# Kernel tuning notes

Hardware: AMD Instinct MI355X
Metric: run time of the kernel (lower is better)

## Reference

```python
import jax, jax.numpy as jnp
import numpy as np

B, T, D = 32, 4096, 768
HEADS, DK, DV = 4, 64, 64
REL_W = 32
HIDDEN = 256


def setup_inputs() -> dict:
    key = jax.random.key(0)
    ks = jax.random.split(key, 12)
    H_sent = jax.random.normal(ks[0], (B, T, D), dtype=jnp.float32)
    # realistic padding: each sample has a random valid length in [2048, T]
    lengths = jax.random.randint(ks[1], (B,), 2048, T + 1)
    attention_mask_sent = (jnp.arange(T)[None, :] < lengths[:, None]).astype(jnp.int32)
    noun_pos = jax.random.randint(ks[2], (B,), 0, 2048).astype(jnp.int32)
    pooled_fields = jax.random.normal(ks[3], (B, D), dtype=jnp.float32)
    # xavier-uniform for (heads, d, dk): fan_in=d, fan_out=dk per torch semantics
    def xavier(k, shape, fan_in, fan_out):
        lim = float(np.sqrt(6.0 / (fan_in + fan_out)))
        return jax.random.uniform(k, shape, jnp.float32, -lim, lim)
    WQ = xavier(ks[4], (HEADS, D, DK), D, DK)
    WK = xavier(ks[5], (HEADS, D, DK), D, DK)
    WV = xavier(ks[6], (HEADS, D, DV), D, DV)
    rel_bias = jnp.zeros((HEADS, 2 * REL_W + 1), jnp.float32) + 0.01 * jax.random.normal(ks[7], (HEADS, 2 * REL_W + 1))
    in_proj = D + HEADS * DV + D  # 1792
    proj_w = xavier(ks[8], (HIDDEN, in_proj), in_proj, HIDDEN)
    proj_b = jnp.zeros((HIDDEN,), jnp.float32)
    mlp_w = xavier(ks[9], (2, HIDDEN), HIDDEN, 2)
    mlp_b = jnp.zeros((2,), jnp.float32)
    return {
        "H_sent": H_sent, "attention_mask_sent": attention_mask_sent,
        "noun_pos": noun_pos, "pooled_fields": pooled_fields,
        "WQ": WQ, "WK": WK, "WV": WV, "rel_bias": rel_bias,
        "proj_w": proj_w, "proj_b": proj_b, "mlp_w": mlp_w, "mlp_b": mlp_b,
    }


def reference(H_sent, attention_mask_sent, noun_pos, pooled_fields,
              WQ, WK, WV, rel_bias, proj_w, proj_b, mlp_w, mlp_b):
    b, t, d = H_sent.shape
    heads, _, dk = WQ.shape
    w = (rel_bias.shape[1] - 1) // 2
    # gather single query vector per sample
    h_i = H_sent[jnp.arange(b), noun_pos]  # (B, d)
    Q = jnp.einsum('bd,hdk->bhk', h_i, WQ)        # (B, H, dk)
    K = jnp.einsum('btd,hdk->bthk', H_sent, WK)   # (B, T, H, dk)
    V = jnp.einsum('btd,hdv->bthv', H_sent, WV)   # (B, T, H, dv)
    scores = jnp.einsum('bhk,bthk->bht', Q, K) / jnp.sqrt(jnp.float32(dk))  # (B,H,T)
    # relative-position bias gathered by clamped delta
    delta = jnp.clip(jnp.arange(t)[None, :] - noun_pos[:, None], -w, w) + w  # (B,T)
    rb = rel_bias[:, delta]                        # (H, B, T)
    scores = scores + jnp.transpose(rb, (1, 0, 2))
    scores = jnp.where(attention_mask_sent[:, None, :] == 0, jnp.float32(-1e9), scores)
    alpha = jax.nn.softmax(scores, axis=-1)        # (B, H, T)
    c = jnp.einsum('bht,bthv->bhv', alpha, V).reshape(b, -1)  # (B, H*dv)
    r = jnp.concatenate([h_i, c, pooled_fields], axis=-1)     # (B, d + H*dv + d)
    hdn = jax.nn.gelu(r @ proj_w.T + proj_b, approximate=False)
    logits = hdn @ mlp_w.T + mlp_b                 # (B, 2)
    return logits
```

## Files before the change

kernel.cpp:

```cpp
#include <hip/hip_runtime.h>
#include <math.h>

#define BB 32
#define TT 4096
#define DD 768
#define NH 4
#define RELW 32
#define NREL 65
#define HIDDEN 256
#define INPROJ 1792

#define NCH 32
#define CROWS (TT / NCH)
#define TROWS 8
#define NT (CROWS / TROWS)
#define C4 (DD / 4)

#define BARRIER() __builtin_amdgcn_s_barrier()
#define FENCE_LGKM() asm volatile("s_waitcnt lgkmcnt(0)" ::: "memory")
#define WAITVM6() asm volatile("s_waitcnt vmcnt(6)" ::: "memory")
#define WAITVM0() asm volatile("s_waitcnt vmcnt(0)" ::: "memory")

__device__ __forceinline__ void gl_lds16(const float* g, float* l) {
    __builtin_amdgcn_global_load_lds(
        (const __attribute__((address_space(1))) float*)(uintptr_t)g,
        (__attribute__((address_space(3))) float*)(uintptr_t)l,
        16, 0, 0);
}

__global__ __launch_bounds__(256) void kA(const float* __restrict__ H,
                                          const int* __restrict__ noun_pos,
                                          const float* __restrict__ WQ,
                                          const float* __restrict__ WK,
                                          float* __restrict__ R,
                                          float* __restrict__ qk_ws) {
    int b = blockIdx.x / NH, h = blockIdx.x % NH;
    __shared__ float hi_s[DD];
    __shared__ float q_s[64];
    int tn = noun_pos[b];
    const float* Hrow = H + ((size_t)b * TT + tn) * DD;
    for (int d = threadIdx.x; d < DD; d += 256) {
        float v = Hrow[d];
        hi_s[d] = v;
        if (h == 0) R[(size_t)b * INPROJ + d] = v;
    }
    __syncthreads();
    if (threadIdx.x < 64) {
        int k = threadIdx.x;
        const float* wq = WQ + (size_t)h * DD * 64 + k;
        float acc = 0.f;
        for (int d = 0; d < DD; ++d) acc += hi_s[d] * wq[(size_t)d * 64];
        q_s[k] = acc;
    }
    __syncthreads();
    for (int d = threadIdx.x; d < DD; d += 256) {
        const float* wk = WK + ((size_t)h * DD + d) * 64;
        float acc = 0.f;
        #pragma unroll
        for (int k = 0; k < 64; ++k) acc += q_s[k] * wk[k];
        qk_ws[((size_t)b * NH + h) * DD + d] = acc * 0.125f;
    }
}

__global__ __launch_bounds__(256, 2) void kFlash(const float* __restrict__ H,
                                                 const int* __restrict__ mask,
                                                 const int* __restrict__ noun_pos,
                                                 const float* __restrict__ rel_bias,
                                                 const float* __restrict__ qk_ws,
                                                 float* __restrict__ macc,
                                                 float* __restrict__ ml) {
    const int b   = blockIdx.x / NCH;
    const int ch  = blockIdx.x % NCH;
    const int tid = threadIdx.x;
    const int wave = tid >> 6, lane = tid & 63;
    const int sl = lane >> 2, hh = lane & 3;

    __shared__ float4 Hts[2][TROWS * C4];
    __shared__ float4 rbL[CROWS];
    __shared__ __align__(16) float sL[TROWS * NH];
    __shared__ int snl;

    const int t0 = ch * CROWS;
    const int tn = noun_pos[b];

    if (tid == 0) snl = 0;
    __syncthreads();

    if (tid < CROWS) {
        int t = t0 + tid;
        int dl = t - tn; dl = dl < -RELW ? -RELW : (dl > RELW ? RELW : dl);
        int mm = mask[(size_t)b * TT + t];
        float4 rv;
        if (mm) {
            rv.x = rel_bias[0 * NREL + dl + RELW];
            rv.y = rel_bias[1 * NREL + dl + RELW];
            rv.z = rel_bias[2 * NREL + dl + RELW];
            rv.w = rel_bias[3 * NREL + dl + RELW];
            atomicMax(&snl, tid + 1);
        } else {
            rv.x = rv.y = rv.z = rv.w = -2.0e9f;
        }
        rbL[tid] = rv;
    }

    float4 qkr[12];
    {
        const float4* qk4 = (const float4*)(qk_ws + ((size_t)b * NH + hh) * DD);
        #pragma unroll
        for (int j = 0; j < 12; ++j) qkr[j] = qk4[j * 16 + sl];
    }

    __syncthreads();
    const int NTE = (snl + TROWS - 1) / TROWS;

    if (NTE == 0) {
        float4 z = {0.f, 0.f, 0.f, 0.f};
        if (tid < C4) {
            float4* mo = (float4*)(macc + (size_t)blockIdx.x * NH * DD);
            mo[0 * C4 + tid] = z; mo[1 * C4 + tid] = z;
            mo[2 * C4 + tid] = z; mo[3 * C4 + tid] = z;
        }
        if (tid == 0) {
            float* mp = ml + (size_t)blockIdx.x * NH * 2;
            mp[0] = -3.0e38f; mp[1] = 0.f; mp[2] = -3.0e38f; mp[3] = 0.f;
            mp[4] = -3.0e38f; mp[5] = 0.f; mp[6] = -3.0e38f; mp[7] = 0.f;
        }
        return;
    }

    float m0 = -3.0e38f, m1 = -3.0e38f, m2 = -3.0e38f, m3 = -3.0e38f;
    float l0 = 0.f, l1 = 0.f, l2 = 0.f, l3 = 0.f;
    float4 a0 = {0.f,0.f,0.f,0.f}, a1 = {0.f,0.f,0.f,0.f};
    float4 a2 = {0.f,0.f,0.f,0.f}, a3 = {0.f,0.f,0.f,0.f};

    const float* Hc = H + ((size_t)b * TT + t0) * DD;

    {
        float* dst = (float*)&Hts[0][0];
        #pragma unroll
        for (int i = 0; i < 6; ++i) {
            int base = (wave * 6 + i) * 256;
            gl_lds16(Hc + base + lane * 4, dst + base);
        }
    }

    #pragma unroll 1
    for (int t = 0; t < NTE; ++t) {
        const int cur = t & 1;
        if (t + 1 < NTE) {
            const float* src = Hc + (size_t)(t + 1) * TROWS * DD;
            float* dst = (float*)&Hts[cur ^ 1][0];
            #pragma unroll
            for (int i = 0; i < 6; ++i) {
                int base = (wave * 6 + i) * 256;
                gl_lds16(src + base + lane * 4, dst + base);
            }
            WAITVM6();
        } else {
            WAITVM0();
        }
        BARRIER();

        const float4* Htc = &Hts[cur][0];
        #pragma unroll
        for (int k = 0; k < 2; ++k) {
            const int r = wave * 2 + k;
            const float4* Hr = Htc + r * C4;
            float acc = 0.f;
            #pragma unroll
            for (int j = 0; j < 12; ++j) {
                float4 hv = Hr[j * 16 + sl];
                acc += hv.x * qkr[j].x + hv.y * qkr[j].y + hv.z * qkr[j].z + hv.w * qkr[j].w;
            }
            acc += __shfl_xor(acc, 4);
            acc += __shfl_xor(acc, 8);
            acc += __shfl_xor(acc, 16);
            acc += __shfl_xor(acc, 32);
            if (lane < NH)
                sL[r * NH + lane] = acc + ((const float*)&rbL[t * TROWS + r])[lane];
        }
        FENCE_LGKM();
        BARRIER();

        float4 p4[TROWS];
        {
            const float4* sL4 = (const float4*)sL;
            #pragma unroll
            for (int r = 0; r < TROWS; ++r) p4[r] = sL4[r];
            float tx = p4[0].x, ty = p4[0].y, tz = p4[0].z, tw = p4[0].w;
            #pragma unroll
            for (int r = 1; r < TROWS; ++r) {
                tx = fmaxf(tx, p4[r].x); ty = fmaxf(ty, p4[r].y);
                tz = fmaxf(tz, p4[r].z); tw = fmaxf(tw, p4[r].w);
            }
            float n0 = fmaxf(m0, tx), n1 = fmaxf(m1, ty);
            float n2 = fmaxf(m2, tz), n3 = fmaxf(m3, tw);
            float s0 = __expf(m0 - n0), s1 = __expf(m1 - n1);
            float s2 = __expf(m2 - n2), s3 = __expf(m3 - n3);
            float q0 = 0.f, q1 = 0.f, q2 = 0.f, q3 = 0.f;
            #pragma unroll
            for (int r = 0; r < TROWS; ++r) {
                p4[r].x = __expf(p4[r].x - n0); q0 += p4[r].x;
                p4[r].y = __expf(p4[r].y - n1); q1 += p4[r].y;
                p4[r].z = __expf(p4[r].z - n2); q2 += p4[r].z;
                p4[r].w = __expf(p4[r].w - n3); q3 += p4[r].w;
            }
            l0 = l0 * s0 + q0; l1 = l1 * s1 + q1;
            l2 = l2 * s2 + q2; l3 = l3 * s3 + q3;
            m0 = n0; m1 = n1; m2 = n2; m3 = n3;
            a0.x *= s0; a0.y *= s0; a0.z *= s0; a0.w *= s0;
            a1.x *= s1; a1.y *= s1; a1.z *= s1; a1.w *= s1;
            a2.x *= s2; a2.y *= s2; a2.z *= s2; a2.w *= s2;
            a3.x *= s3; a3.y *= s3; a3.z *= s3; a3.w *= s3;
        }
        if (tid < C4) {
            #pragma unroll
            for (int r = 0; r < TROWS; ++r) {
                float4 hv = Htc[r * C4 + tid];
                a0.x += p4[r].x * hv.x; a0.y += p4[r].x * hv.y; a0.z += p4[r].x * hv.z; a0.w += p4[r].x * hv.w;
                a1.x += p4[r].y * hv.x; a1.y += p4[r].y * hv.y; a1.z += p4[r].y * hv.z; a1.w += p4[r].y * hv.w;
                a2.x += p4[r].z * hv.x; a2.y += p4[r].z * hv.y; a2.z += p4[r].z * hv.z; a2.w += p4[r].z * hv.w;
                a3.x += p4[r].w * hv.x; a3.y += p4[r].w * hv.y; a3.z += p4[r].w * hv.z; a3.w += p4[r].w * hv.w;
            }
        }
        FENCE_LGKM();
        BARRIER();
    }

    if (tid < C4) {
        float4* mo = (float4*)(macc + (size_t)blockIdx.x * NH * DD);
        mo[0 * C4 + tid] = a0;
        mo[1 * C4 + tid] = a1;
        mo[2 * C4 + tid] = a2;
        mo[3 * C4 + tid] = a3;
    }
    if (tid == 0) {
        float* mp = ml + (size_t)blockIdx.x * NH * 2;
        mp[0] = m0; mp[1] = l0; mp[2] = m1; mp[3] = l1;
        mp[4] = m2; mp[5] = l2; mp[6] = m3; mp[7] = l3;
    }
}

__global__ __launch_bounds__(256) void kT(const float* __restrict__ pw,
                                          float* __restrict__ pwT) {
    int o = blockIdx.x * 256 + threadIdx.x;
    int j = o / INPROJ, i = o % INPROJ;
    pwT[(size_t)i * HIDDEN + j] = pw[o];
}

__global__ __launch_bounds__(256) void kComb(const float* __restrict__ macc,
                                             const float* __restrict__ ml,
                                             float* __restrict__ hbar) {
    int blk = blockIdx.x;
    int b = blk / 12, rem = blk % 12, h = rem / 3, dseg = rem % 3;
    int d = dseg * 256 + threadIdx.x;
    const float* mlb = ml + (size_t)b * NCH * 8 + h * 2;
    float M = -3.0e38f;
    #pragma unroll 8
    for (int c = 0; c < NCH; ++c) M = fmaxf(M, mlb[(size_t)c * 8]);
    float L = 0.f;
    #pragma unroll 8
    for (int c = 0; c < NCH; ++c)
        L += __expf(mlb[(size_t)c * 8] - M) * mlb[(size_t)c * 8 + 1];
    float acc = 0.f;
    const float* mc = macc + ((size_t)b * NCH * NH + h) * DD + d;
    #pragma unroll 8
    for (int c = 0; c < NCH; ++c)
        acc += __expf(mlb[(size_t)c * 8] - M) * mc[(size_t)c * NH * DD];
    hbar[((size_t)b * NH + h) * DD + d] = acc / L;
}

__global__ __launch_bounds__(256) void kC2(const float* __restrict__ hbar,
                                           const float* __restrict__ WV,
                                           const float* __restrict__ pooled,
                                           float* __restrict__ R) {
    int b = blockIdx.x;
    int h = threadIdx.x >> 6, v = threadIdx.x & 63;
    const float* hb = hbar + ((size_t)b * NH + h) * DD;
    const float* wv = WV + (size_t)h * DD * 64 + v;
    float acc = 0.f;
    #pragma unroll 8
    for (int d = 0; d < DD; ++d) acc += hb[d] * wv[(size_t)d * 64];
    R[(size_t)b * INPROJ + DD + threadIdx.x] = acc;
    for (int i = threadIdx.x; i < DD; i += 256)
        R[(size_t)b * INPROJ + DD + 256 + i] = pooled[(size_t)b * DD + i];
}

__global__ __launch_bounds__(256) void kH1(const float* __restrict__ R,
                                           const float* __restrict__ pwT,
                                           float* __restrict__ part2) {
    int b = blockIdx.x / 7, seg = blockIdx.x % 7;
    int j = threadIdx.x;
    __shared__ float r_s[256];
    r_s[j] = R[(size_t)b * INPROJ + seg * 256 + j];
    __syncthreads();
    float acc = 0.f;
    const float* pT = pwT + (size_t)seg * 256 * HIDDEN + j;
    #pragma unroll 8
    for (int i = 0; i < 256; ++i) acc += r_s[i] * pT[(size_t)i * HIDDEN];
    part2[((size_t)b * 7 + seg) * HIDDEN + j] = acc;
}

__global__ __launch_bounds__(256) void kH2(const float* __restrict__ part2,
                                           const float* __restrict__ pb,
                                           const float* __restrict__ mw,
                                           const float* __restrict__ mb,
                                           float* __restrict__ out) {
    int b = blockIdx.x, j = threadIdx.x;
    float acc = pb[j];
    #pragma unroll
    for (int s = 0; s < 7; ++s) acc += part2[((size_t)b * 7 + s) * HIDDEN + j];
    float hdn = 0.5f * acc * (1.f + erff(acc * 0.70710678118654752f));
    float p0 = hdn * mw[j];
    float p1 = hdn * mw[HIDDEN + j];
    #pragma unroll
    for (int off = 32; off; off >>= 1) {
        p0 += __shfl_xor(p0, off);
        p1 += __shfl_xor(p1, off);
    }
    __shared__ float r0[4], r1[4];
    if ((j & 63) == 0) {
        r0[j >> 6] = p0;
        r1[j >> 6] = p1;
    }
    __syncthreads();
    if (j == 0) {
        out[b * 2 + 0] = r0[0] + r0[1] + r0[2] + r0[3] + mb[0];
        out[b * 2 + 1] = r1[0] + r1[1] + r1[2] + r1[3] + mb[1];
    }
}

extern "C" void kernel_launch(void* const* d_in, const int* in_sizes, int n_in,
                              void* d_out, int out_size, void* d_ws, size_t ws_size,
                              hipStream_t stream) {
    const float* H      = (const float*)d_in[0];
    const int*   mask   = (const int*)d_in[1];
    const int*   noun   = (const int*)d_in[2];
    const float* pooled = (const float*)d_in[3];
    const float* WQ     = (const float*)d_in[4];
    const float* WK     = (const float*)d_in[5];
    const float* WV     = (const float*)d_in[6];
    const float* relb   = (const float*)d_in[7];
    const float* pw     = (const float*)d_in[8];
    const float* pb     = (const float*)d_in[9];
    const float* mw     = (const float*)d_in[10];
    const float* mb     = (const float*)d_in[11];
    float* out = (float*)d_out;

    float* ws    = (float*)d_ws;
    float* R     = ws;
    float* qk    = R + (size_t)BB * INPROJ;
    float* macc  = qk + (size_t)BB * NH * DD;
    float* ml    = macc + (size_t)BB * NCH * NH * DD;
    float* hbar  = ml + (size_t)BB * NCH * NH * 2;
    float* pwT   = hbar + (size_t)BB * NH * DD;
    float* part2 = pwT + (size_t)INPROJ * HIDDEN;

    kA<<<BB * NH, 256, 0, stream>>>(H, noun, WQ, WK, R, qk);
    kT<<<(HIDDEN * INPROJ) / 256, 256, 0, stream>>>(pw, pwT);
    kFlash<<<BB * NCH, 256, 0, stream>>>(H, mask, noun, relb, qk, macc, ml);
    kComb<<<BB * 12, 256, 0, stream>>>(macc, ml, hbar);
    kC2<<<BB, 256, 0, stream>>>(hbar, WV, pooled, R);
    kH1<<<BB * 7, 256, 0, stream>>>(R, pwT, part2);
    kH2<<<BB, 256, 0, stream>>>(part2, pb, mw, mb, out);
}
```

Before: 188.7 us.

## Make each wave run independent online softmax over its own rows, merge at end

The flash kernel now has each wave stream its own two rows per tile into its private slice of the shared double buffer. All four heads are computed per row with DPP wave reductions instead of shuffles, and the per-tile block barriers and shared score exchange are gone. Each wave keeps its own max, sum and accumulators with a lazy rescale that only fires when the max grows by more than 8. The four waves are merged through shared memory after the loop. Occupancy hint is raised to 3 blocks per CU. This trades barrier stalls and idle threads for more registers per thread and an extra cross-wave merge step.

```diff
diff --git a/kernel.cpp b/kernel.cpp
--- a/kernel.cpp
+++ b/kernel.cpp
@@ -13,11 +13,8 @@
 #define NCH 32
 #define CROWS (TT / NCH)
 #define TROWS 8
-#define NT (CROWS / TROWS)
 #define C4 (DD / 4)
 
-#define BARRIER() __builtin_amdgcn_s_barrier()
-#define FENCE_LGKM() asm volatile("s_waitcnt lgkmcnt(0)" ::: "memory")
 #define WAITVM6() asm volatile("s_waitcnt vmcnt(6)" ::: "memory")
 #define WAITVM0() asm volatile("s_waitcnt vmcnt(0)" ::: "memory")
 
@@ -26,6 +23,21 @@
         (const __attribute__((address_space(1))) float*)(uintptr_t)g,
         (__attribute__((address_space(3))) float*)(uintptr_t)l,
         16, 0, 0);
+}
+
+template <int CTRL, int RMASK>
+__device__ __forceinline__ float upd0(float x) {
+    return __int_as_float(__builtin_amdgcn_update_dpp(
+        0, __float_as_int(x), CTRL, RMASK, 0xf, true));
+}
+__device__ __forceinline__ float wave_sum64(float x) {
+    x += upd0<0x111, 0xf>(x);
+    x += upd0<0x112, 0xf>(x);
+    x += upd0<0x114, 0xf>(x);
+    x += upd0<0x118, 0xf>(x);
+    x += upd0<0x142, 0xa>(x);
+    x += upd0<0x143, 0xc>(x);
+    return __int_as_float(__builtin_amdgcn_readlane(__float_as_int(x), 63));
 }
 
 __global__ __launch_bounds__(256) void kA(const float* __restrict__ H,
@@ -62,7 +74,30 @@
     }
 }
 
-__global__ __launch_bounds__(256, 2) void kFlash(const float* __restrict__ H,
+#define DOT(ACC, CV, QV) ACC += CV.x*QV.x + CV.y*QV.y + CV.z*QV.z + CV.w*QV.w
+
+#define HUPD(M, L, S0, S1, B0, B1, B2)                                    \
+  {                                                                        \
+    float nm = fmaxf(M, fmaxf(S0, S1));                                    \
+    if (nm > M + 8.0f) {                                                   \
+      float sc = __expf(M - nm);                                           \
+      L *= sc;                                                             \
+      B0.x*=sc; B0.y*=sc; B0.z*=sc; B0.w*=sc;                              \
+      B1.x*=sc; B1.y*=sc; B1.z*=sc; B1.w*=sc;                              \
+      B2.x*=sc; B2.y*=sc; B2.z*=sc; B2.w*=sc;                              \
+      M = nm;                                                              \
+    }                                                                      \
+    float p0 = __expf(S0 - M), p1 = __expf(S1 - M);                        \
+    L += p0 + p1;                                                          \
+    B0.x += p0*c0.x + p1*c3.x; B0.y += p0*c0.y + p1*c3.y;                  \
+    B0.z += p0*c0.z + p1*c3.z; B0.w += p0*c0.w + p1*c3.w;                  \
+    B1.x += p0*c1.x + p1*c4.x; B1.y += p0*c1.y + p1*c4.y;                  \
+    B1.z += p0*c1.z + p1*c4.z; B1.w += p0*c1.w + p1*c4.w;                  \
+    B2.x += p0*c2.x + p1*c5.x; B2.y += p0*c2.y + p1*c5.y;                  \
+    B2.z += p0*c2.z + p1*c5.z; B2.w += p0*c2.w + p1*c5.w;                  \
+  }
+
+__global__ __launch_bounds__(256, 3) void kFlash(const float* __restrict__ H,
                                                  const int* __restrict__ mask,
                                                  const int* __restrict__ noun_pos,
                                                  const float* __restrict__ rel_bias,
@@ -73,11 +108,10 @@
     const int ch  = blockIdx.x % NCH;
     const int tid = threadIdx.x;
     const int wave = tid >> 6, lane = tid & 63;
-    const int sl = lane >> 2, hh = lane & 3;
 
     __shared__ float4 Hts[2][TROWS * C4];
     __shared__ float4 rbL[CROWS];
-    __shared__ __align__(16) float sL[TROWS * NH];
+    __shared__ float mls[4][8];
     __shared__ int snl;
 
     const int t0 = ch * CROWS;
@@ -85,7 +119,6 @@
 
     if (tid == 0) snl = 0;
     __syncthreads();
-
     if (tid < CROWS) {
         int t = t0 + tid;
         int dl = t - tn; dl = dl < -RELW ? -RELW : (dl > RELW ? RELW : dl);
@@ -103,11 +136,14 @@
         rbL[tid] = rv;
     }
 
-    float4 qkr[12];
+    float4 qr[NH][3];
     {
-        const float4* qk4 = (const float4*)(qk_ws + ((size_t)b * NH + hh) * DD);
-        #pragma unroll
-        for (int j = 0; j < 12; ++j) qkr[j] = qk4[j * 16 + sl];
+        const float4* qk4 = (const float4*)(qk_ws + (size_t)b * NH * DD);
+        #pragma unroll
+        for (int h = 0; h < NH; ++h)
+            #pragma unroll
+            for (int j = 0; j < 3; ++j)
+                qr[h][j] = qk4[h * C4 + j * 64 + lane];
     }
 
     __syncthreads();
@@ -115,129 +151,119 @@
 
     if (NTE == 0) {
         float4 z = {0.f, 0.f, 0.f, 0.f};
-        if (tid < C4) {
-            float4* mo = (float4*)(macc + (size_t)blockIdx.x * NH * DD);
-            mo[0 * C4 + tid] = z; mo[1 * C4 + tid] = z;
-            mo[2 * C4 + tid] = z; mo[3 * C4 + tid] = z;
-        }
-        if (tid == 0) {
+        float4* mo = (float4*)(macc + (size_t)blockIdx.x * NH * DD);
+        int h = tid >> 6, ln = tid & 63;
+        #pragma unroll
+        for (int j = 0; j < 3; ++j) mo[h * C4 + j * 64 + ln] = z;
+        if (tid < NH) {
             float* mp = ml + (size_t)blockIdx.x * NH * 2;
-            mp[0] = -3.0e38f; mp[1] = 0.f; mp[2] = -3.0e38f; mp[3] = 0.f;
-            mp[4] = -3.0e38f; mp[5] = 0.f; mp[6] = -3.0e38f; mp[7] = 0.f;
+            mp[tid * 2 + 0] = -3.0e38f; mp[tid * 2 + 1] = 0.f;
         }
         return;
     }
 
     float m0 = -3.0e38f, m1 = -3.0e38f, m2 = -3.0e38f, m3 = -3.0e38f;
     float l0 = 0.f, l1 = 0.f, l2 = 0.f, l3 = 0.f;
-    float4 a0 = {0.f,0.f,0.f,0.f}, a1 = {0.f,0.f,0.f,0.f};
-    float4 a2 = {0.f,0.f,0.f,0.f}, a3 = {0.f,0.f,0.f,0.f};
+    float4 A00{0,0,0,0}, A01{0,0,0,0}, A02{0,0,0,0};
+    float4 A10{0,0,0,0}, A11{0,0,0,0}, A12{0,0,0,0};
+    float4 A20{0,0,0,0}, A21{0,0,0,0}, A22{0,0,0,0};
+    float4 A30{0,0,0,0}, A31{0,0,0,0}, A32{0,0,0,0};
 
     const float* Hc = H + ((size_t)b * TT + t0) * DD;
+    const int woff = wave * 1536;
 
     {
-        float* dst = (float*)&Hts[0][0];
-        #pragma unroll
-        for (int i = 0; i < 6; ++i) {
-            int base = (wave * 6 + i) * 256;
-            gl_lds16(Hc + base + lane * 4, dst + base);
-        }
+        float* dst = (float*)&Hts[0][0] + woff;
+        const float* src = Hc + woff;
+        #pragma unroll
+        for (int i = 0; i < 6; ++i)
+            gl_lds16(src + i * 256 + lane * 4, dst + i * 256);
     }
 
     #pragma unroll 1
     for (int t = 0; t < NTE; ++t) {
         const int cur = t & 1;
         if (t + 1 < NTE) {
-            const float* src = Hc + (size_t)(t + 1) * TROWS * DD;
-            float* dst = (float*)&Hts[cur ^ 1][0];
+            float* dst = (float*)&Hts[cur ^ 1][0] + woff;
+            const float* src = Hc + (size_t)(t + 1) * TROWS * DD + woff;
             #pragma unroll
-            for (int i = 0; i < 6; ++i) {
-                int base = (wave * 6 + i) * 256;
-                gl_lds16(src + base + lane * 4, dst + base);
-            }
+            for (int i = 0; i < 6; ++i)
+                gl_lds16(src + i * 256 + lane * 4, dst + i * 256);
             WAITVM6();
         } else {
             WAITVM0();
         }
-        BARRIER();
-
-        const float4* Htc = &Hts[cur][0];
-        #pragma unroll
-        for (int k = 0; k < 2; ++k) {
-            const int r = wave * 2 + k;
-            const float4* Hr = Htc + r * C4;
-            float acc = 0.f;
-            #pragma unroll
-            for (int j = 0; j < 12; ++j) {
-                float4 hv = Hr[j * 16 + sl];
-                acc += hv.x * qkr[j].x + hv.y * qkr[j].y + hv.z * qkr[j].z + hv.w * qkr[j].w;
-            }
-            acc += __shfl_xor(acc, 4);
-            acc += __shfl_xor(acc, 8);
-            acc += __shfl_xor(acc, 16);
-            acc += __shfl_xor(acc, 32);
-            if (lane < NH)
-                sL[r * NH + lane] = acc + ((const float*)&rbL[t * TROWS + r])[lane];
-        }
-        FENCE_LGKM();
-        BARRIER();
-
-        float4 p4[TROWS];
-        {
-            const float4* sL4 = (const float4*)sL;
-            #pragma unroll
-            for (int r = 0; r < TROWS; ++r) p4[r] = sL4[r];
-            float tx = p4[0].x, ty = p4[0].y, tz = p4[0].z, tw = p4[0].w;
-            #pragma unroll
-            for (int r = 1; r < TROWS; ++r) {
-                tx = fmaxf(tx, p4[r].x); ty = fmaxf(ty, p4[r].y);
-                tz = fmaxf(tz, p4[r].z); tw = fmaxf(tw, p4[r].w);
-            }
-            float n0 = fmaxf(m0, tx), n1 = fmaxf(m1, ty);
-            float n2 = fmaxf(m2, tz), n3 = fmaxf(m3, tw);
-            float s0 = __expf(m0 - n0), s1 = __expf(m1 - n1);
-            float s2 = __expf(m2 - n2), s3 = __expf(m3 - n3);
-            float q0 = 0.f, q1 = 0.f, q2 = 0.f, q3 = 0.f;
-            #pragma unroll
-            for (int r = 0; r < TROWS; ++r) {
-                p4[r].x = __expf(p4[r].x - n0); q0 += p4[r].x;
-                p4[r].y = __expf(p4[r].y - n1); q1 += p4[r].y;
-                p4[r].z = __expf(p4[r].z - n2); q2 += p4[r].z;
-                p4[r].w = __expf(p4[r].w - n3); q3 += p4[r].w;
-            }
-            l0 = l0 * s0 + q0; l1 = l1 * s1 + q1;
-            l2 = l2 * s2 + q2; l3 = l3 * s3 + q3;
-            m0 = n0; m1 = n1; m2 = n2; m3 = n3;
-            a0.x *= s0; a0.y *= s0; a0.z *= s0; a0.w *= s0;
-            a1.x *= s1; a1.y *= s1; a1.z *= s1; a1.w *= s1;
-            a2.x *= s2; a2.y *= s2; a2.z *= s2; a2.w *= s2;
-            a3.x *= s3; a3.y *= s3; a3.z *= s3; a3.w *= s3;
-        }
-        if (tid < C4) {
-            #pragma unroll
-            for (int r = 0; r < TROWS; ++r) {
-                float4 hv = Htc[r * C4 + tid];
-                a0.x += p4[r].x * hv.x; a0.y += p4[r].x * hv.y; a0.z += p4[r].x * hv.z; a0.w += p4[r].x * hv.w;
-                a1.x += p4[r].y * hv.x; a1.y += p4[r].y * hv.y; a1.z += p4[r].y * hv.z; a1.w += p4[r].y * hv.w;
-                a2.x += p4[r].z * hv.x; a2.y += p4[r].z * hv.y; a2.z += p4[r].z * hv.z; a2.w += p4[r].z * hv.w;
-                a3.x += p4[r].w * hv.x; a3.y += p4[r].w * hv.y; a3.z += p4[r].w * hv.z; a3.w += p4[r].w * hv.w;
-            }
-        }
-        FENCE_LGKM();
-        BARRIER();
-    }
-
-    if (tid < C4) {
+        const float4* Hr = &Hts[cur][0] + wave * 384;
+        float4 c0 = Hr[lane],       c1 = Hr[64 + lane],  c2 = Hr[128 + lane];
+        float4 c3 = Hr[192 + lane], c4 = Hr[256 + lane], c5 = Hr[320 + lane];
+
+        float s00 = 0, s01 = 0, s02 = 0, s03 = 0;
+        float s10 = 0, s11 = 0, s12 = 0, s13 = 0;
+        DOT(s00, c0, qr[0][0]); DOT(s00, c1, qr[0][1]); DOT(s00, c2, qr[0][2]);
+        DOT(s01, c0, qr[1][0]); DOT(s01, c1, qr[1][1]); DOT(s01, c2, qr[1][2]);
+        DOT(s02, c0, qr[2][0]); DOT(s02, c1, qr[2][1]); DOT(s02, c2, qr[2][2]);
+        DOT(s03, c0, qr[3][0]); DOT(s03, c1, qr[3][1]); DOT(s03, c2, qr[3][2]);
+        DOT(s10, c3, qr[0][0]); DOT(s10, c4, qr[0][1]); DOT(s10, c5, qr[0][2]);
+        DOT(s11, c3, qr[1][0]); DOT(s11, c4, qr[1][1]); DOT(s11, c5, qr[1][2]);
+        DOT(s12, c3, qr[2][0]); DOT(s12, c4, qr[2][1]); DOT(s12, c5, qr[2][2]);
+        DOT(s13, c3, qr[3][0]); DOT(s13, c4, qr[3][1]); DOT(s13, c5, qr[3][2]);
+        float r00 = wave_sum64(s00), r01 = wave_sum64(s01);
+        float r02 = wave_sum64(s02), r03 = wave_sum64(s03);
+        float r10 = wave_sum64(s10), r11 = wave_sum64(s11);
+        float r12 = wave_sum64(s12), r13 = wave_sum64(s13);
+        float4 rb0 = rbL[t * TROWS + 2 * wave];
+        float4 rb1 = rbL[t * TROWS + 2 * wave + 1];
+        r00 += rb0.x; r01 += rb0.y; r02 += rb0.z; r03 += rb0.w;
+        r10 += rb1.x; r11 += rb1.y; r12 += rb1.z; r13 += rb1.w;
+        HUPD(m0, l0, r00, r10, A00, A01, A02);
+        HUPD(m1, l1, r01, r11, A10, A11, A12);
+        HUPD(m2, l2, r02, r12, A20, A21, A22);
+        HUPD(m3, l3, r03, r13, A30, A31, A32);
+    }
+
+    __syncthreads();
+    float4* scr = &Hts[0][0];
+    #pragma unroll
+    for (int j = 0; j < 3; ++j) {
+        scr[(wave * 4 + 0) * C4 + j * 64 + lane] = j == 0 ? A00 : (j == 1 ? A01 : A02);
+        scr[(wave * 4 + 1) * C4 + j * 64 + lane] = j == 0 ? A10 : (j == 1 ? A11 : A12);
+        scr[(wave * 4 + 2) * C4 + j * 64 + lane] = j == 0 ? A20 : (j == 1 ? A21 : A22);
+        scr[(wave * 4 + 3) * C4 + j * 64 + lane] = j == 0 ? A30 : (j == 1 ? A31 : A32);
+    }
+    if (lane == 0) {
+        mls[wave][0] = m0; mls[wave][1] = l0; mls[wave][2] = m1; mls[wave][3] = l1;
+        mls[wave][4] = m2; mls[wave][5] = l2; mls[wave][6] = m3; mls[wave][7] = l3;
+    }
+    __syncthreads();
+    {
+        int h = tid >> 6, ln = tid & 63;
+        float M = fmaxf(fmaxf(mls[0][h*2], mls[1][h*2]), fmaxf(mls[2][h*2], mls[3][h*2]));
+        float w0 = __expf(mls[0][h*2] - M), w1 = __expf(mls[1][h*2] - M);
+        float w2 = __expf(mls[2][h*2] - M), w3 = __expf(mls[3][h*2] - M);
         float4* mo = (float4*)(macc + (size_t)blockIdx.x * NH * DD);
-        mo[0 * C4 + tid] = a0;
-        mo[1 * C4 + tid] = a1;
-        mo[2 * C4 + tid] = a2;
-        mo[3 * C4 + tid] = a3;
-    }
-    if (tid == 0) {
-        float* mp = ml + (size_t)blockIdx.x * NH * 2;
-        mp[0] = m0; mp[1] = l0; mp[2] = m1; mp[3] = l1;
-        mp[4] = m2; mp[5] = l2; mp[6] = m3; mp[7] = l3;
+        #pragma unroll
+        for (int j = 0; j < 3; ++j) {
+            float4 v0 = scr[(0*4 + h) * C4 + j * 64 + ln];
+            float4 v1 = scr[(1*4 + h) * C4 + j * 64 + ln];
+            float4 v2 = scr[(2*4 + h) * C4 + j * 64 + ln];
+            float4 v3 = scr[(3*4 + h) * C4 + j * 64 + ln];
+            float4 v;
+            v.x = w0*v0.x + w1*v1.x + w2*v2.x + w3*v3.x;
+            v.y = w0*v0.y + w1*v1.y + w2*v2.y + w3*v3.y;
+            v.z = w0*v0.z + w1*v1.z + w2*v2.z + w3*v3.z;
+            v.w = w0*v0.w + w1*v1.w + w2*v2.w + w3*v3.w;
+            mo[h * C4 + j * 64 + ln] = v;
+        }
+        if (tid < NH) {
+            int hh = tid;
+            float Mh = fmaxf(fmaxf(mls[0][hh*2], mls[1][hh*2]), fmaxf(mls[2][hh*2], mls[3][hh*2]));
+            float Lh = __expf(mls[0][hh*2] - Mh) * mls[0][hh*2+1]
+                     + __expf(mls[1][hh*2] - Mh) * mls[1][hh*2+1]
+                     + __expf(mls[2][hh*2] - Mh) * mls[2][hh*2+1]
+                     + __expf(mls[3][hh*2] - Mh) * mls[3][hh*2+1];
+            float* mp = ml + (size_t)blockIdx.x * NH * 2;
+            mp[hh * 2 + 0] = Mh; mp[hh * 2 + 1] = Lh;
+        }
     }
 }
 
```

Result: faster. 152.6 us (-19.1%).
